# Kernel optimization log

Hardware: AMD Instinct MI355X
Metric: run time of the kernel (lower is better)

Reference implementation:

```python
import jax, jax.numpy as jnp
import numpy as np

N_HEAD = 16
DIMS = 1024

def setup_inputs() -> dict:
    key = jax.random.key(0)
    ks = jax.random.split(key, 5)
    B, T, C = 4, 2048, DIMS
    std = 1.0 / np.sqrt(C)
    x = jax.random.normal(ks[0], (B, T, C), dtype=jnp.float32)
    W_attn = jax.random.normal(ks[1], (C, 3 * C), dtype=jnp.float32) * std
    b_attn = jnp.zeros((3 * C,), dtype=jnp.float32)
    W_proj = jax.random.normal(ks[2], (C, C), dtype=jnp.float32) * std
    b_proj = jnp.zeros((C,), dtype=jnp.float32)
    return {"x": x, "W_attn": W_attn, "b_attn": b_attn, "W_proj": W_proj, "b_proj": b_proj}

def reference(x, W_attn, b_attn, W_proj, b_proj):
    B, T, C = x.shape
    H = N_HEAD
    D = C // H
    qkv = x @ W_attn + b_attn  # [B,T,3C]
    q, k, v = jnp.split(qkv, 3, axis=-1)
    # [B,T,C] -> [B,H,T,D]
    q = q.reshape(B, T, H, D).transpose(0, 2, 1, 3)
    k = k.reshape(B, T, H, D).transpose(0, 2, 1, 3)
    v = v.reshape(B, T, H, D).transpose(0, 2, 1, 3)
    att = jnp.einsum('bhqd,bhkd->bhqk', q, k) * (1.0 / np.sqrt(D))
    causal = jnp.tril(jnp.ones((T, T), dtype=bool))  # [T,T]
    att = jnp.where(causal[None, None, :, :], att, -jnp.inf)
    att = jax.nn.softmax(att, axis=-1)
    # dropout p=0.0 -> identity in eval/zero-prob mode
    y = jnp.einsum('bhqk,bhkd->bhqd', att, v)  # [B,H,T,D]
    y = y.transpose(0, 2, 1, 3).reshape(B, T, C)
    y = y @ W_proj + b_proj
    return y
```

## Files before the change

kernel.cpp:

```cpp
#include <hip/hip_runtime.h>
#include <hip/hip_bf16.h>
#include <stdint.h>

typedef unsigned short u16;
typedef unsigned int   u32;

using short8 = __attribute__((ext_vector_type(8))) short;
using f32x4  = __attribute__((ext_vector_type(4))) float;

__device__ __forceinline__ float b2f(u32 u) {
    union { u32 i; float f; } v;
    v.i = u << 16;
    return v.f;
}
__device__ __forceinline__ u16 f2b(float f) {
    union { float f; u32 i; } v; v.f = f;
    u32 x = v.i;
    x += 0x7fffu + ((x >> 16) & 1u);
    return (u16)(x >> 16);
}
__device__ __forceinline__ u32 pkbf16(float lo, float hi) {
    __hip_bfloat162 h = __float22bfloat162_rn(float2{lo, hi});
    return *reinterpret_cast<u32*>(&h);
}
__device__ __forceinline__ float fexp2(float x) {
#if __has_builtin(__builtin_amdgcn_exp2f)
    return __builtin_amdgcn_exp2f(x);
#else
    return exp2f(x);
#endif
}
__device__ __forceinline__ u32 perm_lo(u32 a, u32 b) {
#if __has_builtin(__builtin_amdgcn_perm)
    return __builtin_amdgcn_perm(b, a, 0x05040100u);
#else
    return (a & 0xffffu) | (b << 16);
#endif
}
__device__ __forceinline__ u32 perm_hi(u32 a, u32 b) {
#if __has_builtin(__builtin_amdgcn_perm)
    return __builtin_amdgcn_perm(b, a, 0x07060302u);
#else
    return (a >> 16) | (b & 0xffff0000u);
#endif
}

__device__ __forceinline__ void gll16(const u16* g, u16* l) {
    __builtin_amdgcn_global_load_lds(
        (const __attribute__((address_space(1))) void*)g,
        (__attribute__((address_space(3))) void*)l, 16, 0, 0);
}

__global__ __launch_bounds__(256)
void prep(const float* __restrict__ x, u16* __restrict__ xb,
          const float* __restrict__ Wa, u16* __restrict__ Wta,
          const float* __restrict__ Wp, u16* __restrict__ Wtp)
{
    __shared__ float t[32][33];
    const int bx = blockIdx.x;
    if (bx < 4096) {
        const int i = (bx * 256 + threadIdx.x) * 8;
        const float4 a = *reinterpret_cast<const float4*>(x + i);
        const float4 b = *reinterpret_cast<const float4*>(x + i + 4);
        *reinterpret_cast<uint4*>(xb + i) = make_uint4(
            pkbf16(a.x, a.y), pkbf16(a.z, a.w), pkbf16(b.x, b.y), pkbf16(b.z, b.w));
        return;
    }
    constexpr int R = 1024;
    const int tb = bx - 4096;
    const int cb = tb & 127;
    const int r0 = (tb >> 7) * 32;
    const bool pa = cb < 96;
    const float* W  = pa ? Wa  : Wp;
    u16*         Wt = pa ? Wta : Wtp;
    const int Ncols = pa ? 3072 : 1024;
    const int c0 = (pa ? cb : cb - 96) * 32;
    const int lx = threadIdx.x & 31, ly = threadIdx.x >> 5;
#pragma unroll
    for (int i = 0; i < 4; i++) {
        const int r = ly + i * 8;
        t[r][lx] = W[(size_t)(r0 + r) * Ncols + c0 + lx];
    }
    __syncthreads();
#pragma unroll
    for (int i = 0; i < 4; i++) {
        const int c = ly + i * 8;
        Wt[(size_t)(c0 + c) * R + r0 + lx] = f2b(t[lx][c]);
    }
}

template<typename OT>
__global__ __launch_bounds__(256)
void gemm_mfma(const u16* __restrict__ A, const u16* __restrict__ Bt,
               const float* __restrict__ bias, OT* __restrict__ C,
               int M, int N, int K)
{
    __shared__ u16 As[128 * 32];
    __shared__ u16 Bs[128 * 32];

    const int tid  = threadIdx.x;
    const int w    = tid >> 6;
    const int lane = tid & 63;
    const int quad = lane >> 4;
    const int c16  = lane & 15;
    const int wr   = w >> 1, wc = w & 1;

    const int m0 = blockIdx.y * 128;
    const int n0 = blockIdx.x * 128;

    const int srow = w * 32 + (lane >> 2);
    const int skc  = (lane & 3) * 8;
    const u16* gA = A  + (size_t)(m0 + srow) * K + skc;
    const u16* gB = Bt + (size_t)(n0 + srow) * K + skc;
    u16* lA = As + w * 32 * 32 + lane * 8;
    u16* lB = Bs + w * 32 * 32 + lane * 8;

    f32x4 acc[4][4];
#pragma unroll
    for (int i = 0; i < 4; i++)
#pragma unroll
        for (int j = 0; j < 4; j++) acc[i][j] = (f32x4){0.f, 0.f, 0.f, 0.f};

    for (int k0 = 0; k0 < K; k0 += 32) {
        __syncthreads();
        gll16(gA + k0,                  lA);
        gll16(gA + k0 + 16 * (size_t)K, lA + 16 * 32);
        gll16(gB + k0,                  lB);
        gll16(gB + k0 + 16 * (size_t)K, lB + 16 * 32);
        __syncthreads();

        short8 af[4], bf[4];
#pragma unroll
        for (int i = 0; i < 4; i++)
            af[i] = *reinterpret_cast<const short8*>(&As[(wr * 64 + i * 16 + c16) * 32 + quad * 8]);
#pragma unroll
        for (int j = 0; j < 4; j++)
            bf[j] = *reinterpret_cast<const short8*>(&Bs[(wc * 64 + j * 16 + c16) * 32 + quad * 8]);
#pragma unroll
        for (int i = 0; i < 4; i++)
#pragma unroll
            for (int j = 0; j < 4; j++)
                acc[i][j] = __builtin_amdgcn_mfma_f32_16x16x32_bf16(af[i], bf[j], acc[i][j], 0, 0, 0);
    }

#pragma unroll
    for (int i = 0; i < 4; i++)
#pragma unroll
        for (int j = 0; j < 4; j++) {
            const int colg = n0 + wc * 64 + j * 16 + c16;
            const float bv = bias[colg];
#pragma unroll
            for (int r = 0; r < 4; r++) {
                const int rowg = m0 + wr * 64 + i * 16 + quad * 4 + r;
                const float v = acc[i][j][r] + bv;
                if constexpr (sizeof(OT) == 2)
                    ((u16*)C)[(size_t)rowg * N + colg] = f2b(v);
                else
                    ((float*)C)[(size_t)rowg * N + colg] = v;
            }
        }
}

__global__ __launch_bounds__(512, 2)
void gemm_mfma_256(const u16* __restrict__ A, const u16* __restrict__ Bt,
                   const float* __restrict__ bias, u16* __restrict__ C,
                   int M, int N, int K)
{
    __shared__ u16 ring[4 * 16384];

    const int tid  = threadIdx.x;
    const int w    = tid >> 6;
    const int lane = tid & 63;
    const int quad = lane >> 4;
    const int c16  = lane & 15;
    const int wr   = w >> 2;
    const int wc   = w & 3;

    const int nwg  = gridDim.x * gridDim.y;
    const int orig = blockIdx.y * gridDim.x + blockIdx.x;
    const int swz  = (orig & 7) * (nwg >> 3) + (orig >> 3);
    const int bx   = swz % gridDim.x;
    const int by   = swz / gridDim.x;
    const int m0   = by * 256, n0 = bx * 256;

    const int r0s = w * 16 + (lane >> 2);
    const int qs  = (lane & 3) ^ ((r0s >> 1) & 3);
    const u16* gA = A  + (size_t)(m0 + r0s) * K + qs * 8;
    const u16* gB = Bt + (size_t)(n0 + r0s) * K + qs * 8;
    const size_t hstep = (size_t)128 * K;
    u16* dstB = ring + w * 512 + lane * 8;

    const int slot = quad ^ ((c16 >> 1) & 3);
    const int aoff = (wr * 128 + c16) * 32 + slot * 8;
    const int boff = 8192 + (wc * 64 + c16) * 32 + slot * 8;

    f32x4 acc[8][4];
#pragma unroll
    for (int i = 0; i < 8; i++)
#pragma unroll
        for (int j = 0; j < 4; j++) acc[i][j] = (f32x4){0.f, 0.f, 0.f, 0.f};

    const int nt = K >> 5;

#pragma unroll
    for (int t = 0; t < 3; t++) {
        u16* db = dstB + t * 16384;
        const size_t ko = (size_t)t * 32;
        gll16(gA + ko,         db);
        gll16(gA + ko + hstep, db + 4096);
        gll16(gB + ko,         db + 8192);
        gll16(gB + ko + hstep, db + 12288);
    }

#pragma unroll 1
    for (int t = 0; t < nt; t++) {
        const int remain = nt - 1 - t;
        if (remain >= 2)      asm volatile("s_waitcnt vmcnt(8)" ::: "memory");
        else if (remain == 1) asm volatile("s_waitcnt vmcnt(4)" ::: "memory");
        else                  asm volatile("s_waitcnt vmcnt(0)" ::: "memory");
        asm volatile("s_barrier" ::: "memory");

        const u16* buf = ring + (t & 3) * 16384;
        const bool pf  = (t + 3) < nt;
        u16* db = dstB + ((t + 3) & 3) * 16384;
        const size_t ko = (size_t)(t + 3) * 32;

        short8 bfr[4], afr[4];

#pragma unroll
        for (int j = 0; j < 4; j++)
            bfr[j] = *reinterpret_cast<const short8*>(buf + boff + j * 512);
#pragma unroll
        for (int i = 0; i < 4; i++)
            afr[i] = *reinterpret_cast<const short8*>(buf + aoff + i * 512);
        if (pf) { gll16(gA + ko, db); gll16(gA + ko + hstep, db + 4096); }
        asm volatile("s_waitcnt lgkmcnt(0)" ::: "memory");
        __builtin_amdgcn_sched_barrier(0);
        __builtin_amdgcn_s_setprio(1);
#pragma unroll
        for (int i = 0; i < 4; i++)
#pragma unroll
            for (int j = 0; j < 4; j++)
                acc[i][j] = __builtin_amdgcn_mfma_f32_16x16x32_bf16(afr[i], bfr[j], acc[i][j], 0, 0, 0);
        __builtin_amdgcn_s_setprio(0);
        asm volatile("s_barrier" ::: "memory");

#pragma unroll
        for (int i = 0; i < 4; i++)
            afr[i] = *reinterpret_cast<const short8*>(buf + aoff + (i + 4) * 512);
        if (pf) { gll16(gB + ko, db + 8192); gll16(gB + ko + hstep, db + 12288); }
        asm volatile("s_waitcnt lgkmcnt(0)" ::: "memory");
        __builtin_amdgcn_sched_barrier(0);
        __builtin_amdgcn_s_setprio(1);
#pragma unroll
        for (int i = 0; i < 4; i++)
#pragma unroll
            for (int j = 0; j < 4; j++)
                acc[i + 4][j] = __builtin_amdgcn_mfma_f32_16x16x32_bf16(afr[i], bfr[j], acc[i + 4][j], 0, 0, 0);
        __builtin_amdgcn_s_setprio(0);
        asm volatile("s_barrier" ::: "memory");
    }

    float bv[4];
#pragma unroll
    for (int j = 0; j < 4; j++) bv[j] = bias[n0 + wc * 64 + j * 16 + c16];

    const int erow = wr * 16 + quad * 4;
    const int ecol = wc * 64 + c16;
#pragma unroll
    for (int i = 0; i < 8; i++) {
#pragma unroll
        for (int j = 0; j < 4; j++)
#pragma unroll
            for (int r = 0; r < 4; r++)
                ring[(erow + r) * 264 + ecol + j * 16] = f2b(acc[i][j][r] + bv[j]);
        __syncthreads();
#pragma unroll
        for (int rr = 0; rr < 2; rr++) {
            const int lr = rr * 16 + (tid >> 5);
            const int cc = (tid & 31) * 8;
            const uint4 vvec = *reinterpret_cast<const uint4*>(&ring[lr * 264 + cc]);
            const int gr = m0 + (lr >> 4) * 128 + i * 16 + (lr & 15);
            *reinterpret_cast<uint4*>(&C[(size_t)gr * N + n0 + cc]) = vvec;
        }
        __syncthreads();
    }
}

struct TileState2 {
    f32x4 O[2][4];
    f32x4 lsum[2];
    float m[2];
    short8 qf[2][2];
    int qbase;
};

__device__ __forceinline__ void tile_pass2(
    const u16* __restrict__ Ks, const u16* __restrict__ Vt,
    u16* __restrict__ plrow,
    TileState2& ts, int kt0, int quad, int c16)
{
    const int x7 = c16 & 7;
    const short8 vone = {0x3F80, 0x3F80, 0x3F80, 0x3F80,
                         0x3F80, 0x3F80, 0x3F80, 0x3F80};

    f32x4 s[2][4];
    __builtin_amdgcn_s_setprio(1);
#pragma unroll
    for (int sub = 0; sub < 4; sub++) {
        const int row = sub * 16 + c16;
        short8 kf0 = *reinterpret_cast<const short8*>(&Ks[row * 64 + ((0 + quad) ^ x7) * 8]);
        short8 kf1 = *reinterpret_cast<const short8*>(&Ks[row * 64 + ((4 + quad) ^ x7) * 8]);
        f32x4 a0 = (f32x4){0.f, 0.f, 0.f, 0.f};
        a0 = __builtin_amdgcn_mfma_f32_16x16x32_bf16(kf0, ts.qf[0][0], a0, 0, 0, 0);
        s[0][sub] = __builtin_amdgcn_mfma_f32_16x16x32_bf16(kf1, ts.qf[0][1], a0, 0, 0, 0);
        f32x4 a1 = (f32x4){0.f, 0.f, 0.f, 0.f};
        a1 = __builtin_amdgcn_mfma_f32_16x16x32_bf16(kf0, ts.qf[1][0], a1, 0, 0, 0);
        s[1][sub] = __builtin_amdgcn_mfma_f32_16x16x32_bf16(kf1, ts.qf[1][1], a1, 0, 0, 0);
    }
    __builtin_amdgcn_s_setprio(0);

    short8 pf[2][2];
#pragma unroll
    for (int g = 0; g < 2; g++) {
        const int qg = ts.qbase + g * 16 + c16;
        if (kt0 + 63 > ts.qbase + g * 16) {
#pragma unroll
            for (int sub = 0; sub < 4; sub++)
#pragma unroll
                for (int r = 0; r < 4; r++)
                    if (kt0 + sub * 16 + quad * 4 + r > qg) s[g][sub][r] = -INFINITY;
        }

        float m0a = fmaxf(fmaxf(s[g][0][0], s[g][0][1]), fmaxf(s[g][0][2], s[g][0][3]));
        float m1a = fmaxf(fmaxf(s[g][1][0], s[g][1][1]), fmaxf(s[g][1][2], s[g][1][3]));
        float m2a = fmaxf(fmaxf(s[g][2][0], s[g][2][1]), fmaxf(s[g][2][2], s[g][2][3]));
        float m3a = fmaxf(fmaxf(s[g][3][0], s[g][3][1]), fmaxf(s[g][3][2], s[g][3][3]));
        float mloc = fmaxf(fmaxf(m0a, m1a), fmaxf(m2a, m3a));
        mloc = fmaxf(mloc, __shfl_xor(mloc, 16));
        mloc = fmaxf(mloc, __shfl_xor(mloc, 32));

        if (!__all(mloc <= ts.m[g] + 8.f)) {
            const float mnew = fmaxf(ts.m[g], mloc);
            const float al   = fexp2(ts.m[g] - mnew);
            ts.m[g] = mnew;
#pragma unroll
            for (int r = 0; r < 4; r++) {
                const float alr = __shfl(al, quad * 4 + r);
#pragma unroll
                for (int d = 0; d < 4; d++) ts.O[g][d][r] *= alr;
                ts.lsum[g][r] *= alr;
            }
        }

#pragma unroll
        for (int sub = 0; sub < 4; sub++) {
#pragma unroll
            for (int r = 0; r < 4; r++) s[g][sub][r] = fexp2(s[g][sub][r] - ts.m[g]);
            *reinterpret_cast<uint2*>(
                plrow + c16 * 64 + ((sub * 2 + (quad >> 1)) ^ x7) * 8 + (quad & 1) * 4) =
                make_uint2(pkbf16(s[g][sub][0], s[g][sub][1]), pkbf16(s[g][sub][2], s[g][sub][3]));
        }

#pragma unroll
        for (int c = 0; c < 2; c++)
            pf[g][c] = *reinterpret_cast<const short8*>(
                plrow + c16 * 64 + ((c * 4 + quad) ^ x7) * 8);
    }

    __builtin_amdgcn_s_setprio(1);
#pragma unroll
    for (int dsub = 0; dsub < 4; dsub++) {
        const int row = dsub * 16 + c16;
#pragma unroll
        for (int c = 0; c < 2; c++) {
            short8 vf = *reinterpret_cast<const short8*>(&Vt[row * 64 + ((c * 4 + quad) ^ x7) * 8]);
            ts.O[0][dsub] = __builtin_amdgcn_mfma_f32_16x16x32_bf16(pf[0][c], vf, ts.O[0][dsub], 0, 0, 0);
            ts.O[1][dsub] = __builtin_amdgcn_mfma_f32_16x16x32_bf16(pf[1][c], vf, ts.O[1][dsub], 0, 0, 0);
        }
    }
    ts.lsum[0] = __builtin_amdgcn_mfma_f32_16x16x32_bf16(pf[0][0], vone, ts.lsum[0], 0, 0, 0);
    ts.lsum[0] = __builtin_amdgcn_mfma_f32_16x16x32_bf16(pf[0][1], vone, ts.lsum[0], 0, 0, 0);
    ts.lsum[1] = __builtin_amdgcn_mfma_f32_16x16x32_bf16(pf[1][0], vone, ts.lsum[1], 0, 0, 0);
    ts.lsum[1] = __builtin_amdgcn_mfma_f32_16x16x32_bf16(pf[1][1], vone, ts.lsum[1], 0, 0, 0);
    __builtin_amdgcn_s_setprio(0);
}

__global__ __launch_bounds__(256)
void attn_flash(const u16* __restrict__ qkv, u16* __restrict__ out)
{
    constexpr int T = 2048, C = 1024, C3 = 3072;

    __shared__ u16 Ks[2][64 * 64];
    __shared__ u16 Vt[2][64 * 64];
    __shared__ u16 Pl[4][16 * 64];

    const int tid  = threadIdx.x;
    const int w    = tid >> 6;
    const int lane = tid & 63;
    const int quad = lane >> 4;
    const int c16  = lane & 15;

    const int flat = blockIdx.y * gridDim.x + blockIdx.x;
    const int xcd  = flat & 7;
    const int tt   = flat >> 3;
    const int qp   = tt & 7;
    const int bh   = ((tt >> 3) << 3) | xcd;
    const int qtA  = qp;
    const int qtB  = 15 - qp;
    const int h    = bh & 15;
    const int b    = bh >> 4;

    const int kr  = tid >> 2, kq = tid & 3;
    const int vkp = tid & 31, vdg = (tid >> 5) * 8;
    const u16* baseK = qkv + (size_t)(b * T + kr) * C3 + C + h * 64 + kq * 16;
    const u16* baseV = qkv + (size_t)(b * T + 2 * vkp) * C3 + 2 * C + h * 64 + vdg;

    const int kx  = kr & 7;
    const int kd0 = kr * 64 + ((2 * kq + 0) ^ kx) * 8;
    const int kd1 = kr * 64 + ((2 * kq + 1) ^ kx) * 8;
    const int vslot = vkp >> 2, vintra = (vkp & 3) * 2;

    u16* plrow = &Pl[w][0];

    uint4 ka, kb, va, vb;

#pragma unroll 1
    for (int phase = 0; phase < 2; ++phase) {
        const int qt = phase ? qtA : qtB;

        TileState2 ts;
        ts.qbase = qt * 128 + w * 32;
        ts.m[0] = ts.m[1] = -INFINITY;
        ts.lsum[0] = ts.lsum[1] = (f32x4){0.f, 0.f, 0.f, 0.f};
#pragma unroll
        for (int g = 0; g < 2; g++)
#pragma unroll
            for (int d = 0; d < 4; d++) ts.O[g][d] = (f32x4){0.f, 0.f, 0.f, 0.f};
        constexpr float QSCALE = 0.125f * 1.44269504089f;
#pragma unroll
        for (int g = 0; g < 2; g++)
#pragma unroll
            for (int c = 0; c < 2; c++) {
                short8 rq = *reinterpret_cast<const short8*>(
                    qkv + (size_t)(b * T + ts.qbase + g * 16 + c16) * C3 + h * 64 + c * 32 + quad * 8);
#pragma unroll
                for (int j = 0; j < 8; j++)
                    ts.qf[g][c][j] = (short)f2b(b2f((u16)rq[j]) * QSCALE);
            }

        const int ktmax = 2 * qt + 1;
        const int qwmax = ts.qbase + 31;

        {
            const uint4* gp = reinterpret_cast<const uint4*>(baseK);
            ka = gp[0]; kb = gp[1];
            va = *reinterpret_cast<const uint4*>(baseV);
            vb = *reinterpret_cast<const uint4*>(baseV + C3);
        }
        __syncthreads();
        {
            *reinterpret_cast<uint4*>(&Ks[0][kd0]) = ka;
            *reinterpret_cast<uint4*>(&Ks[0][kd1]) = kb;
            const u32* aw = reinterpret_cast<const u32*>(&va);
            const u32* bw = reinterpret_cast<const u32*>(&vb);
#pragma unroll
            for (int i = 0; i < 4; i++) {
                const int d0 = vdg + 2 * i;
                *reinterpret_cast<u32*>(&Vt[0][d0 * 64 + (vslot ^ (2 * i)) * 8 + vintra]) =
                    perm_lo(aw[i], bw[i]);
                *reinterpret_cast<u32*>(&Vt[0][(d0 + 1) * 64 + (vslot ^ (2 * i + 1)) * 8 + vintra]) =
                    perm_hi(aw[i], bw[i]);
            }
        }

        for (int kt = 0; kt <= ktmax; kt++) {
            const int cur = kt & 1;
            __syncthreads();

            if (kt < ktmax) {
                const int nk0 = (kt + 1) * 64;
                const uint4* gp = reinterpret_cast<const uint4*>(baseK + (size_t)nk0 * C3);
                ka = gp[0]; kb = gp[1];
                const u16* g0 = baseV + (size_t)nk0 * C3;
                va = *reinterpret_cast<const uint4*>(g0);
                vb = *reinterpret_cast<const uint4*>(g0 + C3);
            }

            if (kt * 64 <= qwmax)
                tile_pass2(Ks[cur], Vt[cur], plrow, ts, kt * 64, quad, c16);

            if (kt < ktmax) {
                const int nxt = cur ^ 1;
                *reinterpret_cast<uint4*>(&Ks[nxt][kd0]) = ka;
                *reinterpret_cast<uint4*>(&Ks[nxt][kd1]) = kb;
                const u32* aw = reinterpret_cast<const u32*>(&va);
                const u32* bw = reinterpret_cast<const u32*>(&vb);
#pragma unroll
                for (int i = 0; i < 4; i++) {
                    const int d0 = vdg + 2 * i;
                    *reinterpret_cast<u32*>(&Vt[nxt][d0 * 64 + (vslot ^ (2 * i)) * 8 + vintra]) =
                        perm_lo(aw[i], bw[i]);
                    *reinterpret_cast<u32*>(&Vt[nxt][(d0 + 1) * 64 + (vslot ^ (2 * i + 1)) * 8 + vintra]) =
                        perm_hi(aw[i], bw[i]);
                }
            }
        }

#pragma unroll
        for (int g = 0; g < 2; g++) {
#pragma unroll
            for (int r = 0; r < 4; r++) {
                const float invr = 1.0f / ts.lsum[g][r];
                const int qrow = ts.qbase + g * 16 + quad * 4 + r;
#pragma unroll
                for (int dsub = 0; dsub < 4; dsub++)
                    out[(size_t)(b * T + qrow) * C + h * 64 + dsub * 16 + c16] =
                        f2b(ts.O[g][dsub][r] * invr);
            }
        }
    }
}

extern "C" void kernel_launch(void* const* d_in, const int* in_sizes, int n_in,
                              void* d_out, int out_size, void* d_ws, size_t ws_size,
                              hipStream_t stream)
{
    constexpr int B = 4, T = 2048, C = 1024;
    constexpr int M = B * T;
    const float* x      = (const float*)d_in[0];
    const float* W_attn = (const float*)d_in[1];
    const float* b_attn = (const float*)d_in[2];
    const float* W_proj = (const float*)d_in[3];
    const float* b_proj = (const float*)d_in[4];
    float* out = (float*)d_out;

    char* p = (char*)d_ws;
    u16* qkv     = (u16*)p;                 p += (size_t)M * 3 * C * sizeof(u16);
    u16* xb      = (u16*)p;
    u16* attn_o  = (u16*)p;                 p += (size_t)M * C * sizeof(u16);
    u16* Wt_attn = (u16*)p;                 p += (size_t)3 * C * C * sizeof(u16);
    u16* Wt_proj = (u16*)p;

    prep<<<dim3(8192), 256, 0, stream>>>(x, xb, W_attn, Wt_attn, W_proj, Wt_proj);

    gemm_mfma_256<<<dim3(3 * C / 256, M / 256), 512, 0, stream>>>(
        xb, Wt_attn, b_attn, qkv, M, 3 * C, C);

    attn_flash<<<dim3(8, B * 16), 256, 0, stream>>>(qkv, attn_o);

    gemm_mfma<float><<<dim3(C / 128, M / 128), 256, 0, stream>>>(
        attn_o, Wt_proj, b_proj, out, M, C, C);
}
```

Before: 268.0 us.

## Pipeline output projection GEMM with 4-stage LDS ring; compute softmax row sums with VALU

Measured after the change: 260.6 us. 1.03x faster.

```diff
diff --git a/kernel.cpp b/kernel.cpp
--- a/kernel.cpp
+++ b/kernel.cpp
@@ -89,78 +89,6 @@
     }
 }
 
-template<typename OT>
-__global__ __launch_bounds__(256)
-void gemm_mfma(const u16* __restrict__ A, const u16* __restrict__ Bt,
-               const float* __restrict__ bias, OT* __restrict__ C,
-               int M, int N, int K)
-{
-    __shared__ u16 As[128 * 32];
-    __shared__ u16 Bs[128 * 32];
-
-    const int tid  = threadIdx.x;
-    const int w    = tid >> 6;
-    const int lane = tid & 63;
-    const int quad = lane >> 4;
-    const int c16  = lane & 15;
-    const int wr   = w >> 1, wc = w & 1;
-
-    const int m0 = blockIdx.y * 128;
-    const int n0 = blockIdx.x * 128;
-
-    const int srow = w * 32 + (lane >> 2);
-    const int skc  = (lane & 3) * 8;
-    const u16* gA = A  + (size_t)(m0 + srow) * K + skc;
-    const u16* gB = Bt + (size_t)(n0 + srow) * K + skc;
-    u16* lA = As + w * 32 * 32 + lane * 8;
-    u16* lB = Bs + w * 32 * 32 + lane * 8;
-
-    f32x4 acc[4][4];
-#pragma unroll
-    for (int i = 0; i < 4; i++)
-#pragma unroll
-        for (int j = 0; j < 4; j++) acc[i][j] = (f32x4){0.f, 0.f, 0.f, 0.f};
-
-    for (int k0 = 0; k0 < K; k0 += 32) {
-        __syncthreads();
-        gll16(gA + k0,                  lA);
-        gll16(gA + k0 + 16 * (size_t)K, lA + 16 * 32);
-        gll16(gB + k0,                  lB);
-        gll16(gB + k0 + 16 * (size_t)K, lB + 16 * 32);
-        __syncthreads();
-
-        short8 af[4], bf[4];
-#pragma unroll
-        for (int i = 0; i < 4; i++)
-            af[i] = *reinterpret_cast<const short8*>(&As[(wr * 64 + i * 16 + c16) * 32 + quad * 8]);
-#pragma unroll
-        for (int j = 0; j < 4; j++)
-            bf[j] = *reinterpret_cast<const short8*>(&Bs[(wc * 64 + j * 16 + c16) * 32 + quad * 8]);
-#pragma unroll
-        for (int i = 0; i < 4; i++)
-#pragma unroll
-            for (int j = 0; j < 4; j++)
-                acc[i][j] = __builtin_amdgcn_mfma_f32_16x16x32_bf16(af[i], bf[j], acc[i][j], 0, 0, 0);
-    }
-
-#pragma unroll
-    for (int i = 0; i < 4; i++)
-#pragma unroll
-        for (int j = 0; j < 4; j++) {
-            const int colg = n0 + wc * 64 + j * 16 + c16;
-            const float bv = bias[colg];
-#pragma unroll
-            for (int r = 0; r < 4; r++) {
-                const int rowg = m0 + wr * 64 + i * 16 + quad * 4 + r;
-                const float v = acc[i][j][r] + bv;
-                if constexpr (sizeof(OT) == 2)
-                    ((u16*)C)[(size_t)rowg * N + colg] = f2b(v);
-                else
-                    ((float*)C)[(size_t)rowg * N + colg] = v;
-            }
-        }
-}
-
 __global__ __launch_bounds__(512, 2)
 void gemm_mfma_256(const u16* __restrict__ A, const u16* __restrict__ Bt,
                    const float* __restrict__ bias, u16* __restrict__ C,
@@ -287,10 +215,112 @@
     }
 }
 
+__global__ __launch_bounds__(512, 2)
+void gemm_mfma_256x128(const u16* __restrict__ A, const u16* __restrict__ Bt,
+                       const float* __restrict__ bias, float* __restrict__ C,
+                       int M, int N, int K)
+{
+    __shared__ u16 ring[4 * 12288];
+
+    const int tid  = threadIdx.x;
+    const int w    = tid >> 6;
+    const int lane = tid & 63;
+    const int quad = lane >> 4;
+    const int c16  = lane & 15;
+    const int wr   = w >> 1;
+    const int wc   = w & 1;
+
+    const int nwg  = gridDim.x * gridDim.y;
+    const int orig = blockIdx.y * gridDim.x + blockIdx.x;
+    const int swz  = (orig & 7) * (nwg >> 3) + (orig >> 3);
+    const int bx   = swz % gridDim.x;
+    const int by   = swz / gridDim.x;
+    const int m0   = by * 256, n0 = bx * 128;
+
+    const int r0s = tid >> 2;
+    const int qs  = (tid & 3) ^ ((r0s >> 1) & 3);
+    const u16* gA = A  + (size_t)(m0 + r0s) * K + qs * 8;
+    const u16* gB = Bt + (size_t)(n0 + r0s) * K + qs * 8;
+    const size_t hstep = (size_t)128 * K;
+    u16* dstB = ring + tid * 8;
+
+    const int slot = quad ^ ((c16 >> 1) & 3);
+    const int aoff = (wr * 64 + c16) * 32 + slot * 8;
+    const int boff = 8192 + (wc * 64 + c16) * 32 + slot * 8;
+
+    f32x4 acc[4][4];
+#pragma unroll
+    for (int i = 0; i < 4; i++)
+#pragma unroll
+        for (int j = 0; j < 4; j++) acc[i][j] = (f32x4){0.f, 0.f, 0.f, 0.f};
+
+    const int nt = K >> 5;
+
+#pragma unroll
+    for (int t = 0; t < 3; t++) {
+        u16* db = dstB + t * 12288;
+        const size_t ko = (size_t)t * 32;
+        gll16(gA + ko,         db);
+        gll16(gA + ko + hstep, db + 4096);
+        gll16(gB + ko,         db + 8192);
+    }
+
+#pragma unroll 1
+    for (int t = 0; t < nt; t++) {
+        const int remain = nt - 1 - t;
+        if (remain >= 2)      asm volatile("s_waitcnt vmcnt(6)" ::: "memory");
+        else if (remain == 1) asm volatile("s_waitcnt vmcnt(3)" ::: "memory");
+        else                  asm volatile("s_waitcnt vmcnt(0)" ::: "memory");
+        asm volatile("s_barrier" ::: "memory");
+
+        const u16* buf = ring + (t & 3) * 12288;
+        const bool pf  = (t + 3) < nt;
+        u16* db = dstB + ((t + 3) & 3) * 12288;
+        const size_t ko = (size_t)(t + 3) * 32;
+
+        short8 afr[4], bfr[4];
+#pragma unroll
+        for (int j = 0; j < 4; j++)
+            bfr[j] = *reinterpret_cast<const short8*>(buf + boff + j * 512);
+#pragma unroll
+        for (int i = 0; i < 4; i++)
+            afr[i] = *reinterpret_cast<const short8*>(buf + aoff + i * 512);
+        if (pf) {
+            gll16(gA + ko,         db);
+            gll16(gA + ko + hstep, db + 4096);
+            gll16(gB + ko,         db + 8192);
+        }
+        asm volatile("s_waitcnt lgkmcnt(0)" ::: "memory");
+        __builtin_amdgcn_sched_barrier(0);
+        __builtin_amdgcn_s_setprio(1);
+#pragma unroll
+        for (int i = 0; i < 4; i++)
+#pragma unroll
+            for (int j = 0; j < 4; j++)
+                acc[i][j] = __builtin_amdgcn_mfma_f32_16x16x32_bf16(afr[i], bfr[j], acc[i][j], 0, 0, 0);
+        __builtin_amdgcn_s_setprio(0);
+        asm volatile("s_barrier" ::: "memory");
+    }
+
+    float bv[4];
+#pragma unroll
+    for (int j = 0; j < 4; j++) bv[j] = bias[n0 + wc * 64 + j * 16 + c16];
+#pragma unroll
+    for (int i = 0; i < 4; i++)
+#pragma unroll
+        for (int j = 0; j < 4; j++) {
+            const int colg = n0 + wc * 64 + j * 16 + c16;
+#pragma unroll
+            for (int r = 0; r < 4; r++) {
+                const int rowg = m0 + wr * 64 + i * 16 + quad * 4 + r;
+                C[(size_t)rowg * N + colg] = acc[i][j][r] + bv[j];
+            }
+        }
+}
+
 struct TileState2 {
     f32x4 O[2][4];
-    f32x4 lsum[2];
-    float m[2];
+    float m[2], l[2];
     short8 qf[2][2];
     int qbase;
 };
@@ -301,8 +331,6 @@
     TileState2& ts, int kt0, int quad, int c16)
 {
     const int x7 = c16 & 7;
-    const short8 vone = {0x3F80, 0x3F80, 0x3F80, 0x3F80,
-                         0x3F80, 0x3F80, 0x3F80, 0x3F80};
 
     f32x4 s[2][4];
     __builtin_amdgcn_s_setprio(1);
@@ -344,23 +372,26 @@
             const float mnew = fmaxf(ts.m[g], mloc);
             const float al   = fexp2(ts.m[g] - mnew);
             ts.m[g] = mnew;
+            ts.l[g] *= al;
 #pragma unroll
             for (int r = 0; r < 4; r++) {
                 const float alr = __shfl(al, quad * 4 + r);
 #pragma unroll
                 for (int d = 0; d < 4; d++) ts.O[g][d][r] *= alr;
-                ts.lsum[g][r] *= alr;
-            }
-        }
-
+            }
+        }
+
+        float ls = 0.f;
 #pragma unroll
         for (int sub = 0; sub < 4; sub++) {
 #pragma unroll
             for (int r = 0; r < 4; r++) s[g][sub][r] = fexp2(s[g][sub][r] - ts.m[g]);
+            ls += (s[g][sub][0] + s[g][sub][1]) + (s[g][sub][2] + s[g][sub][3]);
             *reinterpret_cast<uint2*>(
                 plrow + c16 * 64 + ((sub * 2 + (quad >> 1)) ^ x7) * 8 + (quad & 1) * 4) =
                 make_uint2(pkbf16(s[g][sub][0], s[g][sub][1]), pkbf16(s[g][sub][2], s[g][sub][3]));
         }
+        ts.l[g] += ls;
 
 #pragma unroll
         for (int c = 0; c < 2; c++)
@@ -379,10 +410,6 @@
             ts.O[1][dsub] = __builtin_amdgcn_mfma_f32_16x16x32_bf16(pf[1][c], vf, ts.O[1][dsub], 0, 0, 0);
         }
     }
-    ts.lsum[0] = __builtin_amdgcn_mfma_f32_16x16x32_bf16(pf[0][0], vone, ts.lsum[0], 0, 0, 0);
-    ts.lsum[0] = __builtin_amdgcn_mfma_f32_16x16x32_bf16(pf[0][1], vone, ts.lsum[0], 0, 0, 0);
-    ts.lsum[1] = __builtin_amdgcn_mfma_f32_16x16x32_bf16(pf[1][0], vone, ts.lsum[1], 0, 0, 0);
-    ts.lsum[1] = __builtin_amdgcn_mfma_f32_16x16x32_bf16(pf[1][1], vone, ts.lsum[1], 0, 0, 0);
     __builtin_amdgcn_s_setprio(0);
 }
 
@@ -432,7 +459,7 @@
         TileState2 ts;
         ts.qbase = qt * 128 + w * 32;
         ts.m[0] = ts.m[1] = -INFINITY;
-        ts.lsum[0] = ts.lsum[1] = (f32x4){0.f, 0.f, 0.f, 0.f};
+        ts.l[0] = ts.l[1] = 0.f;
 #pragma unroll
         for (int g = 0; g < 2; g++)
 #pragma unroll
@@ -509,9 +536,13 @@
 
 #pragma unroll
         for (int g = 0; g < 2; g++) {
+            float ls = ts.l[g];
+            ls += __shfl_xor(ls, 16);
+            ls += __shfl_xor(ls, 32);
+            const float inv = 1.0f / ls;
 #pragma unroll
             for (int r = 0; r < 4; r++) {
-                const float invr = 1.0f / ts.lsum[g][r];
+                const float invr = __shfl(inv, quad * 4 + r);
                 const int qrow = ts.qbase + g * 16 + quad * 4 + r;
 #pragma unroll
                 for (int dsub = 0; dsub < 4; dsub++)
@@ -549,6 +580,6 @@
 
     attn_flash<<<dim3(8, B * 16), 256, 0, stream>>>(qkv, attn_o);
 
-    gemm_mfma<float><<<dim3(C / 128, M / 128), 256, 0, stream>>>(
+    gemm_mfma_256x128<<<dim3(C / 128, M / 256), 512, 0, stream>>>(
         attn_o, Wt_proj, b_proj, out, M, C, C);
 }
```
